# Kernel optimization log

Hardware: AMD Instinct MI355X
Metric: run time of the kernel (lower is better)

The kernel has to match this reference:

```python
import jax, jax.numpy as jnp
import numpy as np

EPS = 1e-5
GROUPS = 32
N_HEADS = 8
HEAD_DIM = 64


def setup_inputs() -> dict:
    key = jax.random.key(0)
    ks = jax.random.split(key, 8)
    b, c, d, w, hs = 2, 512, 16, 16, 16
    ctx_len, ctx_dim = 1024, 768
    inner = N_HEADS * HEAD_DIM  # 512
    return {
        "x": jax.random.normal(ks[0], (b, c, d, w, hs), jnp.float32),
        "context": jax.random.normal(ks[1], (b, ctx_len, ctx_dim), jnp.float32),
        "gamma": jnp.ones((c,), jnp.float32),
        "beta": jnp.zeros((c,), jnp.float32),
        "Wq": jax.random.normal(ks[2], (c, inner), jnp.float32) * (c ** -0.5),
        "Wk": jax.random.normal(ks[3], (ctx_dim, inner), jnp.float32) * (ctx_dim ** -0.5),
        "Wv": jax.random.normal(ks[4], (ctx_dim, inner), jnp.float32) * (ctx_dim ** -0.5),
        "Wo": jax.random.normal(ks[5], (inner, c), jnp.float32) * (inner ** -0.5),
        "bo": jnp.zeros((c,), jnp.float32),
    }


def reference(x, context, gamma, beta, Wq, Wk, Wv, Wo, bo):
    b, c, d, w, hs = x.shape
    n = d * w * hs  # sequence length of voxel tokens
    scale = HEAD_DIM ** -0.5

    # GroupNorm over (channels-in-group, spatial)
    xg = x.reshape(b, GROUPS, -1)
    mu = jnp.mean(xg, axis=-1, keepdims=True)
    var = jnp.mean(jnp.square(xg - mu), axis=-1, keepdims=True)
    xn = (xg - mu) * jax.lax.rsqrt(var + EPS)
    xn = xn.reshape(b, c, n) * gamma[None, :, None] + beta[None, :, None]

    x_seq = jnp.swapaxes(x.reshape(b, c, n), 1, 2)   # [b, n, c] residual
    xn_seq = jnp.swapaxes(xn, 1, 2)                   # [b, n, c]

    q = (xn_seq @ Wq).reshape(b, n, N_HEADS, HEAD_DIM)
    k = (context @ Wk).reshape(b, -1, N_HEADS, HEAD_DIM)
    v = (context @ Wv).reshape(b, -1, N_HEADS, HEAD_DIM)

    attn = jax.nn.softmax(jnp.einsum('bqhd,bkhd->bhqk', q, k) * scale, axis=-1)
    out = jnp.einsum('bhqk,bkhd->bqhd', attn, v).reshape(b, n, N_HEADS * HEAD_DIM)

    out = out @ Wo + bo  # dropout is identity in eval mode
    out = out + x_seq
    return jnp.swapaxes(out, 1, 2).reshape(b, c, d, w, hs)
```

## Files before the change

### kernel.cpp

```cpp
#include <hip/hip_runtime.h>
#include <hip/hip_bf16.h>

#define B 2
#define C 512
#define NTOK 4096
#define GROUPS 32
#define CPG 16
#define CTX 1024
#define CDIM 768
#define NH 8
#define HD 64
#define INNER 512
#define EPS 1e-5f
#define KVBLK 64
#define NCH (CTX / KVBLK)

typedef unsigned short bf16_t;
typedef __attribute__((ext_vector_type(8))) short bf16x8;
typedef __attribute__((ext_vector_type(4))) float f32x4;

__device__ __forceinline__ bf16_t f2b(float f) {
    unsigned u = __float_as_uint(f);
    u += 0x7fffu + ((u >> 16) & 1u);
    return (bf16_t)(u >> 16);
}

__device__ __forceinline__ int swz(int row, int col) {
    return row * 64 + (col ^ ((row & 7) << 3));
}

__global__ __launch_bounds__(256) void gn_partial_kernel(const float* __restrict__ x,
                                                         float2* __restrict__ partials) {
    int blk = blockIdx.x;
    const float* base = x + (size_t)blk * 4096;
    float s = 0.f, ss = 0.f;
    #pragma unroll
    for (int i = 0; i < 4; ++i) {
        float4 v = *(const float4*)&base[(threadIdx.x + i * 256) * 4];
        s += v.x + v.y + v.z + v.w;
        ss += v.x * v.x + v.y * v.y + v.z * v.z + v.w * v.w;
    }
    #pragma unroll
    for (int o = 32; o > 0; o >>= 1) { s += __shfl_xor(s, o); ss += __shfl_xor(ss, o); }
    __shared__ float ls[2][4];
    int wv = threadIdx.x >> 6, ln = threadIdx.x & 63;
    if (ln == 0) { ls[0][wv] = s; ls[1][wv] = ss; }
    __syncthreads();
    if (threadIdx.x == 0) {
        partials[blk] = make_float2(ls[0][0] + ls[0][1] + ls[0][2] + ls[0][3],
                                    ls[1][0] + ls[1][1] + ls[1][2] + ls[1][3]);
    }
}

__global__ __launch_bounds__(64) void gn_finalize_kernel(const float2* __restrict__ partials,
                                                         float* __restrict__ stats) {
    int g = threadIdx.x;
    float s = 0.f, ss = 0.f;
    #pragma unroll
    for (int i = 0; i < 16; ++i) {
        float2 p = partials[g * 16 + i];
        s += p.x; ss += p.y;
    }
    float mu = s / (float)(CPG * NTOK);
    float var = ss / (float)(CPG * NTOK) - mu * mu;
    stats[g] = mu;
    stats[64 + g] = rsqrtf(var + EPS);
}

__global__ __launch_bounds__(256) void gn_apply_kernel(const float* __restrict__ x,
                                                       const float* __restrict__ stats,
                                                       const float* __restrict__ gamma,
                                                       const float* __restrict__ beta,
                                                       bf16_t* __restrict__ xn) {
    __shared__ float tile[32][33];
    int b = blockIdx.z;
    int c0 = blockIdx.y * 32;
    int t0 = blockIdx.x * 32;
    int tt = threadIdx.x & 31, cr = threadIdx.x >> 5;
    #pragma unroll
    for (int i = 0; i < 4; ++i) {
        int c = c0 + cr + 8 * i;
        float mu = stats[b * 32 + (c >> 4)];
        float rs = stats[64 + b * 32 + (c >> 4)];
        float v = x[((size_t)(b * C + c)) * NTOK + t0 + tt];
        tile[cr + 8 * i][tt] = (v - mu) * rs * gamma[c] + beta[c];
    }
    __syncthreads();
    #pragma unroll
    for (int i = 0; i < 4; ++i) {
        int t = t0 + cr + 8 * i;
        int c = c0 + tt;
        xn[((size_t)b * NTOK + t) * C + c] = f2b(tile[tt][cr + 8 * i]);
    }
}

__global__ __launch_bounds__(256) void wcast_kernel(const float* __restrict__ in,
                                                    bf16_t* __restrict__ out,
                                                    int K, int N, int ldo) {
    __shared__ float t[32][33];
    int k0 = blockIdx.x * 32, n0 = blockIdx.y * 32;
    int xx = threadIdx.x & 31, yy = threadIdx.x >> 5;
    #pragma unroll
    for (int i = 0; i < 4; ++i)
        t[yy + 8 * i][xx] = in[(size_t)(k0 + yy + 8 * i) * N + n0 + xx];
    __syncthreads();
    #pragma unroll
    for (int i = 0; i < 4; ++i)
        out[(size_t)(n0 + yy + 8 * i) * ldo + k0 + xx] = f2b(t[xx][yy + 8 * i]);
}

__global__ __launch_bounds__(256) void castctx_kernel(const float* __restrict__ in,
                                                      bf16_t* __restrict__ out) {
    int i = (blockIdx.x * 256 + threadIdx.x) * 4;
    float4 v = *(const float4*)&in[i];
    out[i + 0] = f2b(v.x); out[i + 1] = f2b(v.y);
    out[i + 2] = f2b(v.z); out[i + 3] = f2b(v.w);
}

__global__ __launch_bounds__(256) void gemm_qkv_kernel(
    const bf16_t* __restrict__ A, const bf16_t* __restrict__ Bt,
    bf16_t* __restrict__ outK, bf16_t* __restrict__ outV,
    int K, int seqshift, float oscale, int vtrans) {
    __shared__ __align__(16) bf16_t As[64][40];
    __shared__ __align__(16) bf16_t Bs[64][40];
    const int tid = threadIdx.x;
    const int l = tid & 63, w = tid >> 6;
    const int wr = w >> 1, wc = w & 1;
    const int lg = l >> 4, lr = l & 15;
    const int m0 = blockIdx.x * 64, n0 = blockIdx.y * 64;
    const int rowS = tid >> 2, c8 = (tid & 3) * 8;
    const bf16_t* pa = A  + (size_t)(m0 + rowS) * K + c8;
    const bf16_t* pb = Bt + (size_t)(n0 + rowS) * K + c8;
    f32x4 acc[2][2] = {};
    float4 ra = *(const float4*)pa;
    float4 rb = *(const float4*)pb;
    *(float4*)&As[rowS][c8] = ra;
    *(float4*)&Bs[rowS][c8] = rb;
    for (int k0 = 0; k0 < K; k0 += 32) {
        __syncthreads();
        if (k0 + 32 < K) {
            ra = *(const float4*)(pa + k0 + 32);
            rb = *(const float4*)(pb + k0 + 32);
        }
        bf16x8 af[2], bfm[2];
        af[0]  = *(bf16x8*)&As[wr * 32 + lr][lg * 8];
        af[1]  = *(bf16x8*)&As[wr * 32 + 16 + lr][lg * 8];
        bfm[0] = *(bf16x8*)&Bs[wc * 32 + lr][lg * 8];
        bfm[1] = *(bf16x8*)&Bs[wc * 32 + 16 + lr][lg * 8];
        #pragma unroll
        for (int mi = 0; mi < 2; ++mi)
            #pragma unroll
            for (int ni = 0; ni < 2; ++ni)
                acc[mi][ni] = __builtin_amdgcn_mfma_f32_16x16x32_bf16(af[mi], bfm[ni], acc[mi][ni], 0, 0, 0);
        __syncthreads();
        if (k0 + 32 < K) {
            *(float4*)&As[rowS][c8] = ra;
            *(float4*)&Bs[rowS][c8] = rb;
        }
    }
    const int seqmask = (1 << seqshift) - 1;
    #pragma unroll
    for (int ni = 0; ni < 2; ++ni) {
        int n = n0 + wc * 32 + ni * 16 + lr;
        int nn = n & (INNER - 1);
        int h = nn >> 6, dd = nn & 63;
        bool isV = (n >= INNER);
        #pragma unroll
        for (int mi = 0; mi < 2; ++mi) {
            int mb = m0 + wr * 32 + mi * 16 + lg * 4;
            int bidx = mb >> seqshift, seqb = mb & seqmask;
            if (isV && vtrans) {
                ushort4 pv;
                pv.x = f2b(acc[mi][ni][0] * oscale);
                pv.y = f2b(acc[mi][ni][1] * oscale);
                pv.z = f2b(acc[mi][ni][2] * oscale);
                pv.w = f2b(acc[mi][ni][3] * oscale);
                *(ushort4*)&outV[((size_t)(bidx * NH + h) * HD + dd) * (size_t)(seqmask + 1) + seqb] = pv;
            } else {
                bf16_t* dst = isV ? outV : outK;
                #pragma unroll
                for (int r = 0; r < 4; ++r)
                    dst[(((size_t)(bidx * NH + h) << seqshift) + seqb + r) * HD + dd] =
                        f2b(acc[mi][ni][r] * oscale);
            }
        }
    }
}

__global__ __launch_bounds__(256) void gemm_o_kernel(
    const bf16_t* __restrict__ A, const bf16_t* __restrict__ Bt,
    const float* __restrict__ bo, const float* __restrict__ x,
    float* __restrict__ out) {
    __shared__ __align__(16) bf16_t As[64][40];
    __shared__ __align__(16) bf16_t Bs[64][40];
    const int tid = threadIdx.x;
    const int l = tid & 63, w = tid >> 6;
    const int wr = w >> 1, wc = w & 1;
    const int lg = l >> 4, lr = l & 15;
    const int m0 = blockIdx.x * 64, n0 = blockIdx.y * 64;
    const int rowS = tid >> 2, c8 = (tid & 3) * 8;
    const bf16_t* pa = A  + (size_t)(m0 + rowS) * INNER + c8;
    const bf16_t* pb = Bt + (size_t)(n0 + rowS) * INNER + c8;
    f32x4 acc[2][2] = {};
    float4 ra = *(const float4*)pa;
    float4 rb = *(const float4*)pb;
    *(float4*)&As[rowS][c8] = ra;
    *(float4*)&Bs[rowS][c8] = rb;
    for (int k0 = 0; k0 < INNER; k0 += 32) {
        __syncthreads();
        if (k0 + 32 < INNER) {
            ra = *(const float4*)(pa + k0 + 32);
            rb = *(const float4*)(pb + k0 + 32);
        }
        bf16x8 af[2], bfm[2];
        af[0]  = *(bf16x8*)&As[wr * 32 + lr][lg * 8];
        af[1]  = *(bf16x8*)&As[wr * 32 + 16 + lr][lg * 8];
        bfm[0] = *(bf16x8*)&Bs[wc * 32 + lr][lg * 8];
        bfm[1] = *(bf16x8*)&Bs[wc * 32 + 16 + lr][lg * 8];
        #pragma unroll
        for (int mi = 0; mi < 2; ++mi)
            #pragma unroll
            for (int ni = 0; ni < 2; ++ni)
                acc[mi][ni] = __builtin_amdgcn_mfma_f32_16x16x32_bf16(af[mi], bfm[ni], acc[mi][ni], 0, 0, 0);
        __syncthreads();
        if (k0 + 32 < INNER) {
            *(float4*)&As[rowS][c8] = ra;
            *(float4*)&Bs[rowS][c8] = rb;
        }
    }
    #pragma unroll
    for (int mi = 0; mi < 2; ++mi) {
        int mb = m0 + wr * 32 + mi * 16 + lg * 4;
        int t = mb & (NTOK - 1);
        int bb = mb >> 12;
        #pragma unroll
        for (int ni = 0; ni < 2; ++ni) {
            int cc = n0 + wc * 32 + ni * 16 + lr;
            size_t o = (((size_t)(bb * C + cc)) << 12) + t;
            float4 xr = *(const float4*)&x[o];
            float bias = bo[cc];
            float4 ov;
            ov.x = acc[mi][ni][0] + bias + xr.x;
            ov.y = acc[mi][ni][1] + bias + xr.y;
            ov.z = acc[mi][ni][2] + bias + xr.z;
            ov.w = acc[mi][ni][3] + bias + xr.w;
            *(float4*)&out[o] = ov;
        }
    }
}

__global__ __launch_bounds__(256) void attn_kernel(
    const bf16_t* __restrict__ Q, const bf16_t* __restrict__ Kb,
    const bf16_t* __restrict__ Vt, bf16_t* __restrict__ AO) {
    __shared__ __align__(16) bf16_t Ks[64 * 64];
    __shared__ __align__(16) bf16_t Vs[64 * 64];
    __shared__ __align__(16) bf16_t Ps[4][32 * 64];
    const int tid = threadIdx.x;
    const int l = tid & 63, w = tid >> 6;
    const int lg = l >> 4, lr = l & 15;
    const int bh = blockIdx.x >> 5;
    const int tile = blockIdx.x & 31;
    const int b = bh >> 3, h = bh & 7;
    const int t0 = tile * 128 + w * 32;

    bf16x8 qf[2][2];
    #pragma unroll
    for (int mi = 0; mi < 2; ++mi) {
        const bf16_t* qb = Q + ((size_t)bh * NTOK + t0 + mi * 16 + lr) * HD;
        qf[mi][0] = *(const bf16x8*)&qb[lg * 8];
        qf[mi][1] = *(const bf16x8*)&qb[32 + lg * 8];
    }

    f32x4 acc[2][4] = {};
    float mrow[2][4], lrow[2][4];
    #pragma unroll
    for (int mi = 0; mi < 2; ++mi)
        #pragma unroll
        for (int r = 0; r < 4; ++r) { mrow[mi][r] = -1e30f; lrow[mi][r] = 0.f; }

    const bf16_t* kbase = Kb + (size_t)bh * CTX * HD;
    const bf16_t* vbase = Vt + (size_t)bh * HD * CTX;
    const int srow = tid >> 3, sc8 = (tid & 7) * 8;

    float4 kr0 = *(const float4*)&kbase[(size_t)srow * HD + sc8];
    float4 kr1 = *(const float4*)&kbase[(size_t)(srow + 32) * HD + sc8];
    float4 vr0 = *(const float4*)&vbase[(size_t)srow * CTX + sc8];
    float4 vr1 = *(const float4*)&vbase[(size_t)(srow + 32) * CTX + sc8];
    *(float4*)&Ks[swz(srow, sc8)] = kr0;
    *(float4*)&Ks[swz(srow + 32, sc8)] = kr1;
    *(float4*)&Vs[swz(srow, sc8)] = vr0;
    *(float4*)&Vs[swz(srow + 32, sc8)] = vr1;

    for (int c = 0; c < NCH; ++c) {
        __syncthreads();
        if (c + 1 < NCH) {
            int k1 = (c + 1) * KVBLK;
            kr0 = *(const float4*)&kbase[(size_t)(k1 + srow) * HD + sc8];
            kr1 = *(const float4*)&kbase[(size_t)(k1 + srow + 32) * HD + sc8];
            vr0 = *(const float4*)&vbase[(size_t)srow * CTX + k1 + sc8];
            vr1 = *(const float4*)&vbase[(size_t)(srow + 32) * CTX + k1 + sc8];
        }
        f32x4 sf[2][4] = {};
        #pragma unroll
        for (int ks = 0; ks < 2; ++ks)
            #pragma unroll
            for (int ni = 0; ni < 4; ++ni) {
                bf16x8 kf = *(bf16x8*)&Ks[swz(ni * 16 + lr, ks * 32 + lg * 8)];
                sf[0][ni] = __builtin_amdgcn_mfma_f32_16x16x32_bf16(qf[0][ks], kf, sf[0][ni], 0, 0, 0);
                sf[1][ni] = __builtin_amdgcn_mfma_f32_16x16x32_bf16(qf[1][ks], kf, sf[1][ni], 0, 0, 0);
            }
        #pragma unroll
        for (int mi = 0; mi < 2; ++mi)
            #pragma unroll
            for (int r = 0; r < 4; ++r) {
                float s0 = sf[mi][0][r], s1 = sf[mi][1][r];
                float s2 = sf[mi][2][r], s3 = sf[mi][3][r];
                float cm = fmaxf(fmaxf(s0, s1), fmaxf(s2, s3));
                cm = fmaxf(cm, __shfl_xor(cm, 1));
                cm = fmaxf(cm, __shfl_xor(cm, 2));
                cm = fmaxf(cm, __shfl_xor(cm, 4));
                cm = fmaxf(cm, __shfl_xor(cm, 8));
                float mn = fmaxf(mrow[mi][r], cm);
                float scl = __expf(mrow[mi][r] - mn);
                float p0 = __expf(s0 - mn), p1 = __expf(s1 - mn);
                float p2 = __expf(s2 - mn), p3 = __expf(s3 - mn);
                float rs = p0 + p1 + p2 + p3;
                rs += __shfl_xor(rs, 1); rs += __shfl_xor(rs, 2);
                rs += __shfl_xor(rs, 4); rs += __shfl_xor(rs, 8);
                lrow[mi][r] = lrow[mi][r] * scl + rs;
                mrow[mi][r] = mn;
                #pragma unroll
                for (int ni = 0; ni < 4; ++ni) acc[mi][ni][r] *= scl;
                int prow = mi * 16 + lg * 4 + r;
                Ps[w][swz(prow, 0 * 16 + lr)] = f2b(p0);
                Ps[w][swz(prow, 1 * 16 + lr)] = f2b(p1);
                Ps[w][swz(prow, 2 * 16 + lr)] = f2b(p2);
                Ps[w][swz(prow, 3 * 16 + lr)] = f2b(p3);
            }
        #pragma unroll
        for (int ks = 0; ks < 2; ++ks) {
            bf16x8 pf0 = *(bf16x8*)&Ps[w][swz(lr, ks * 32 + lg * 8)];
            bf16x8 pf1 = *(bf16x8*)&Ps[w][swz(16 + lr, ks * 32 + lg * 8)];
            #pragma unroll
            for (int ni = 0; ni < 4; ++ni) {
                bf16x8 vf = *(bf16x8*)&Vs[swz(ni * 16 + lr, ks * 32 + lg * 8)];
                acc[0][ni] = __builtin_amdgcn_mfma_f32_16x16x32_bf16(pf0, vf, acc[0][ni], 0, 0, 0);
                acc[1][ni] = __builtin_amdgcn_mfma_f32_16x16x32_bf16(pf1, vf, acc[1][ni], 0, 0, 0);
            }
        }
        __syncthreads();
        if (c + 1 < NCH) {
            *(float4*)&Ks[swz(srow, sc8)] = kr0;
            *(float4*)&Ks[swz(srow + 32, sc8)] = kr1;
            *(float4*)&Vs[swz(srow, sc8)] = vr0;
            *(float4*)&Vs[swz(srow + 32, sc8)] = vr1;
        }
    }

    #pragma unroll
    for (int mi = 0; mi < 2; ++mi)
        #pragma unroll
        for (int ni = 0; ni < 4; ++ni)
            #pragma unroll
            for (int r = 0; r < 4; ++r) {
                int t = t0 + mi * 16 + lg * 4 + r;
                AO[((size_t)b * NTOK + t) * INNER + h * HD + ni * 16 + lr] =
                    f2b(acc[mi][ni][r] / lrow[mi][r]);
            }
}

extern "C" void kernel_launch(void* const* d_in, const int* in_sizes, int n_in,
                              void* d_out, int out_size, void* d_ws, size_t ws_size,
                              hipStream_t stream) {
    const float* x       = (const float*)d_in[0];
    const float* context = (const float*)d_in[1];
    const float* gamma   = (const float*)d_in[2];
    const float* beta    = (const float*)d_in[3];
    const float* Wq      = (const float*)d_in[4];
    const float* Wk      = (const float*)d_in[5];
    const float* Wv      = (const float*)d_in[6];
    const float* Wo      = (const float*)d_in[7];
    const float* bo      = (const float*)d_in[8];
    float* out = (float*)d_out;

    char* p = (char*)d_ws;
    float* stats = (float*)p;            p += 1024;
    float2* parts = (float2*)p;          p += 1024 * sizeof(float2);
    bf16_t* xn   = (bf16_t*)p;           p += (size_t)B * NTOK * C * 2;
    bf16_t* ctxb = (bf16_t*)p;           p += (size_t)B * CTX * CDIM * 2;
    bf16_t* Wqt  = (bf16_t*)p;           p += (size_t)INNER * C * 2;
    bf16_t* Wkvt = (bf16_t*)p;           p += (size_t)2 * INNER * CDIM * 2;
    bf16_t* Wot  = (bf16_t*)p;           p += (size_t)C * INNER * 2;
    bf16_t* qb   = (bf16_t*)p;           p += (size_t)B * NH * NTOK * HD * 2;
    bf16_t* kb   = (bf16_t*)p;           p += (size_t)B * NH * CTX * HD * 2;
    bf16_t* vb   = (bf16_t*)p;           p += (size_t)B * NH * CTX * HD * 2;
    bf16_t* ao   = (bf16_t*)p;           p += (size_t)B * NTOK * INNER * 2;

    hipLaunchKernelGGL(gn_partial_kernel, dim3(1024), dim3(256), 0, stream, x, parts);
    hipLaunchKernelGGL(gn_finalize_kernel, dim3(1), dim3(64), 0, stream, parts, stats);
    hipLaunchKernelGGL(gn_apply_kernel, dim3(NTOK / 32, C / 32, B), dim3(256), 0, stream,
                       x, stats, gamma, beta, xn);
    hipLaunchKernelGGL(wcast_kernel, dim3(16, 16), dim3(256), 0, stream, Wq, Wqt, C, INNER, C);
    hipLaunchKernelGGL(wcast_kernel, dim3(24, 16), dim3(256), 0, stream, Wk, Wkvt, CDIM, INNER, CDIM);
    hipLaunchKernelGGL(wcast_kernel, dim3(24, 16), dim3(256), 0, stream,
                       Wv, Wkvt + (size_t)INNER * CDIM, CDIM, INNER, CDIM);
    hipLaunchKernelGGL(wcast_kernel, dim3(16, 16), dim3(256), 0, stream, Wo, Wot, INNER, C, INNER);
    hipLaunchKernelGGL(castctx_kernel, dim3(B * CTX * CDIM / 1024), dim3(256), 0, stream,
                       context, ctxb);
    hipLaunchKernelGGL(gemm_qkv_kernel, dim3(128, 8), dim3(256), 0, stream,
                       xn, Wqt, qb, qb, C, 12, 0.125f, 0);
    hipLaunchKernelGGL(gemm_qkv_kernel, dim3(32, 16), dim3(256), 0, stream,
                       ctxb, Wkvt, kb, vb, CDIM, 10, 1.0f, 1);
    hipLaunchKernelGGL(attn_kernel, dim3(B * NH * (NTOK / 128)), dim3(256), 0, stream,
                       qb, kb, vb, ao);
    hipLaunchKernelGGL(gemm_o_kernel, dim3(128, 8), dim3(256), 0, stream,
                       ao, Wot, bo, x, out);
}
```

Before: 201.8 us.

## Fuse GN finalize, batch weight casts, cast context in GEMM, shrink attention tiles

The GroupNorm finalize step now runs inside the apply kernel, the four weight-cast launches become one launch, and the context fp32→bf16 cast is done inside the K/V GEMM's A-tile load, which drops two launches and an intermediate buffer. The attention kernel is reworked so each wave handles 16 query rows instead of 32, doubling the grid and halving registers and P scratch. Softmax now uses exp2 with log2e folded into the Q scale. The exchange is more redundant K/V tile loading per query and extra conversion work inside the GEMM loop.

```diff
diff --git a/kernel.cpp b/kernel.cpp
--- a/kernel.cpp
+++ b/kernel.cpp
@@ -14,6 +14,7 @@
 #define EPS 1e-5f
 #define KVBLK 64
 #define NCH (CTX / KVBLK)
+#define LOG2E 1.44269504f
 
 typedef unsigned short bf16_t;
 typedef __attribute__((ext_vector_type(8))) short bf16x8;
@@ -23,6 +24,13 @@
     unsigned u = __float_as_uint(f);
     u += 0x7fffu + ((u >> 16) & 1u);
     return (bf16_t)(u >> 16);
+}
+
+__device__ __forceinline__ float4 pack8(const float* v) {
+    union { ushort s[8]; float4 f; } u;
+    #pragma unroll
+    for (int j = 0; j < 8; ++j) u.s[j] = f2b(v[j]);
+    return u.f;
 }
 
 __device__ __forceinline__ int swz(int row, int col) {
@@ -52,38 +60,39 @@
     }
 }
 
-__global__ __launch_bounds__(64) void gn_finalize_kernel(const float2* __restrict__ partials,
-                                                         float* __restrict__ stats) {
-    int g = threadIdx.x;
-    float s = 0.f, ss = 0.f;
-    #pragma unroll
-    for (int i = 0; i < 16; ++i) {
-        float2 p = partials[g * 16 + i];
-        s += p.x; ss += p.y;
-    }
-    float mu = s / (float)(CPG * NTOK);
-    float var = ss / (float)(CPG * NTOK) - mu * mu;
-    stats[g] = mu;
-    stats[64 + g] = rsqrtf(var + EPS);
-}
-
 __global__ __launch_bounds__(256) void gn_apply_kernel(const float* __restrict__ x,
-                                                       const float* __restrict__ stats,
+                                                       const float2* __restrict__ partials,
                                                        const float* __restrict__ gamma,
                                                        const float* __restrict__ beta,
                                                        bf16_t* __restrict__ xn) {
     __shared__ float tile[32][33];
+    __shared__ float gmu[2], grs[2];
     int b = blockIdx.z;
     int c0 = blockIdx.y * 32;
     int t0 = blockIdx.x * 32;
-    int tt = threadIdx.x & 31, cr = threadIdx.x >> 5;
+    int tid = threadIdx.x;
+    if (tid < 32) {
+        int gi = tid >> 4, pi = tid & 15;
+        float2 pp = partials[b * C + c0 + gi * 16 + pi];
+        float s = pp.x, ss = pp.y;
+        #pragma unroll
+        for (int o = 8; o > 0; o >>= 1) { s += __shfl_xor(s, o); ss += __shfl_xor(ss, o); }
+        if (pi == 0) {
+            float mu = s / (float)(CPG * NTOK);
+            float var = ss / (float)(CPG * NTOK) - mu * mu;
+            gmu[gi] = mu;
+            grs[gi] = rsqrtf(var + EPS);
+        }
+    }
+    int tt = tid & 31, cr = tid >> 5;
+    __syncthreads();
     #pragma unroll
     for (int i = 0; i < 4; ++i) {
-        int c = c0 + cr + 8 * i;
-        float mu = stats[b * 32 + (c >> 4)];
-        float rs = stats[64 + b * 32 + (c >> 4)];
+        int co = cr + 8 * i;
+        int c = c0 + co;
+        float mu = gmu[co >> 4], rs = grs[co >> 4];
         float v = x[((size_t)(b * C + c)) * NTOK + t0 + tt];
-        tile[cr + 8 * i][tt] = (v - mu) * rs * gamma[c] + beta[c];
+        tile[co][tt] = (v - mu) * rs * gamma[c] + beta[c];
     }
     __syncthreads();
     #pragma unroll
@@ -94,31 +103,32 @@
     }
 }
 
-__global__ __launch_bounds__(256) void wcast_kernel(const float* __restrict__ in,
-                                                    bf16_t* __restrict__ out,
-                                                    int K, int N, int ldo) {
+__global__ __launch_bounds__(256) void wcast_all_kernel(
+    const float* __restrict__ Wq, const float* __restrict__ Wk,
+    const float* __restrict__ Wv, const float* __restrict__ Wo,
+    bf16_t* __restrict__ Wqt, bf16_t* __restrict__ Wkvt, bf16_t* __restrict__ Wot) {
+    int z = blockIdx.z;
+    const float* in; bf16_t* out; int K;
+    if (z == 0)      { in = Wq; out = Wqt;  K = C; }
+    else if (z == 1) { in = Wk; out = Wkvt; K = CDIM; }
+    else if (z == 2) { in = Wv; out = Wkvt + (size_t)INNER * CDIM; K = CDIM; }
+    else             { in = Wo; out = Wot;  K = INNER; }
+    int k0 = blockIdx.x * 32, n0 = blockIdx.y * 32;
+    if (k0 >= K) return;
     __shared__ float t[32][33];
-    int k0 = blockIdx.x * 32, n0 = blockIdx.y * 32;
     int xx = threadIdx.x & 31, yy = threadIdx.x >> 5;
     #pragma unroll
     for (int i = 0; i < 4; ++i)
-        t[yy + 8 * i][xx] = in[(size_t)(k0 + yy + 8 * i) * N + n0 + xx];
+        t[yy + 8 * i][xx] = in[(size_t)(k0 + yy + 8 * i) * INNER + n0 + xx];
     __syncthreads();
     #pragma unroll
     for (int i = 0; i < 4; ++i)
-        out[(size_t)(n0 + yy + 8 * i) * ldo + k0 + xx] = f2b(t[xx][yy + 8 * i]);
-}
-
-__global__ __launch_bounds__(256) void castctx_kernel(const float* __restrict__ in,
-                                                      bf16_t* __restrict__ out) {
-    int i = (blockIdx.x * 256 + threadIdx.x) * 4;
-    float4 v = *(const float4*)&in[i];
-    out[i + 0] = f2b(v.x); out[i + 1] = f2b(v.y);
-    out[i + 2] = f2b(v.z); out[i + 3] = f2b(v.w);
-}
-
+        out[(size_t)(n0 + yy + 8 * i) * K + k0 + xx] = f2b(t[xx][yy + 8 * i]);
+}
+
+template <int AFP32>
 __global__ __launch_bounds__(256) void gemm_qkv_kernel(
-    const bf16_t* __restrict__ A, const bf16_t* __restrict__ Bt,
+    const void* __restrict__ Av, const bf16_t* __restrict__ Bt,
     bf16_t* __restrict__ outK, bf16_t* __restrict__ outV,
     int K, int seqshift, float oscale, int vtrans) {
     __shared__ __align__(16) bf16_t As[64][40];
@@ -129,17 +139,32 @@
     const int lg = l >> 4, lr = l & 15;
     const int m0 = blockIdx.x * 64, n0 = blockIdx.y * 64;
     const int rowS = tid >> 2, c8 = (tid & 3) * 8;
-    const bf16_t* pa = A  + (size_t)(m0 + rowS) * K + c8;
+    const bf16_t* pa16 = AFP32 ? nullptr : (const bf16_t*)Av + (size_t)(m0 + rowS) * K + c8;
+    const float*  pa32 = AFP32 ? (const float*)Av + (size_t)(m0 + rowS) * K + c8 : nullptr;
     const bf16_t* pb = Bt + (size_t)(n0 + rowS) * K + c8;
     f32x4 acc[2][2] = {};
-    float4 ra = *(const float4*)pa;
-    float4 rb = *(const float4*)pb;
+    float av[8];
+    float4 ra, rb;
+    if (AFP32) {
+        *(float4*)&av[0] = *(const float4*)pa32;
+        *(float4*)&av[4] = *(const float4*)(pa32 + 4);
+        ra = pack8(av);
+    } else {
+        ra = *(const float4*)pa16;
+    }
+    rb = *(const float4*)pb;
     *(float4*)&As[rowS][c8] = ra;
     *(float4*)&Bs[rowS][c8] = rb;
     for (int k0 = 0; k0 < K; k0 += 32) {
         __syncthreads();
         if (k0 + 32 < K) {
-            ra = *(const float4*)(pa + k0 + 32);
+            if (AFP32) {
+                *(float4*)&av[0] = *(const float4*)(pa32 + k0 + 32);
+                *(float4*)&av[4] = *(const float4*)(pa32 + k0 + 36);
+                ra = pack8(av);
+            } else {
+                ra = *(const float4*)(pa16 + k0 + 32);
+            }
             rb = *(const float4*)(pb + k0 + 32);
         }
         bf16x8 af[2], bfm[2];
@@ -254,29 +279,24 @@
     const bf16_t* __restrict__ Vt, bf16_t* __restrict__ AO) {
     __shared__ __align__(16) bf16_t Ks[64 * 64];
     __shared__ __align__(16) bf16_t Vs[64 * 64];
-    __shared__ __align__(16) bf16_t Ps[4][32 * 64];
+    __shared__ __align__(16) bf16_t Ps[4][16 * 64];
     const int tid = threadIdx.x;
     const int l = tid & 63, w = tid >> 6;
     const int lg = l >> 4, lr = l & 15;
-    const int bh = blockIdx.x >> 5;
-    const int tile = blockIdx.x & 31;
+    const int bh = blockIdx.x >> 6;
+    const int tile = blockIdx.x & 63;
     const int b = bh >> 3, h = bh & 7;
-    const int t0 = tile * 128 + w * 32;
-
-    bf16x8 qf[2][2];
-    #pragma unroll
-    for (int mi = 0; mi < 2; ++mi) {
-        const bf16_t* qb = Q + ((size_t)bh * NTOK + t0 + mi * 16 + lr) * HD;
-        qf[mi][0] = *(const bf16x8*)&qb[lg * 8];
-        qf[mi][1] = *(const bf16x8*)&qb[32 + lg * 8];
-    }
-
-    f32x4 acc[2][4] = {};
-    float mrow[2][4], lrow[2][4];
-    #pragma unroll
-    for (int mi = 0; mi < 2; ++mi)
-        #pragma unroll
-        for (int r = 0; r < 4; ++r) { mrow[mi][r] = -1e30f; lrow[mi][r] = 0.f; }
+    const int t0 = tile * 64 + w * 16;
+
+    const bf16_t* qbase = Q + ((size_t)bh * NTOK + t0 + lr) * HD;
+    bf16x8 qf[2];
+    qf[0] = *(const bf16x8*)&qbase[lg * 8];
+    qf[1] = *(const bf16x8*)&qbase[32 + lg * 8];
+
+    f32x4 acc[4] = {};
+    float mrow[4], lrow[4];
+    #pragma unroll
+    for (int r = 0; r < 4; ++r) { mrow[r] = -1e30f; lrow[r] = 0.f; }
 
     const bf16_t* kbase = Kb + (size_t)bh * CTX * HD;
     const bf16_t* vbase = Vt + (size_t)bh * HD * CTX;
@@ -300,52 +320,49 @@
             vr0 = *(const float4*)&vbase[(size_t)srow * CTX + k1 + sc8];
             vr1 = *(const float4*)&vbase[(size_t)(srow + 32) * CTX + k1 + sc8];
         }
-        f32x4 sf[2][4] = {};
+        f32x4 sf[4] = {};
         #pragma unroll
         for (int ks = 0; ks < 2; ++ks)
             #pragma unroll
             for (int ni = 0; ni < 4; ++ni) {
                 bf16x8 kf = *(bf16x8*)&Ks[swz(ni * 16 + lr, ks * 32 + lg * 8)];
-                sf[0][ni] = __builtin_amdgcn_mfma_f32_16x16x32_bf16(qf[0][ks], kf, sf[0][ni], 0, 0, 0);
-                sf[1][ni] = __builtin_amdgcn_mfma_f32_16x16x32_bf16(qf[1][ks], kf, sf[1][ni], 0, 0, 0);
+                sf[ni] = __builtin_amdgcn_mfma_f32_16x16x32_bf16(qf[ks], kf, sf[ni], 0, 0, 0);
             }
         #pragma unroll
-        for (int mi = 0; mi < 2; ++mi)
+        for (int r = 0; r < 4; ++r) {
+            float s0 = sf[0][r], s1 = sf[1][r];
+            float s2 = sf[2][r], s3 = sf[3][r];
+            float cm = fmaxf(fmaxf(s0, s1), fmaxf(s2, s3));
+            cm = fmaxf(cm, __shfl_xor(cm, 1));
+            cm = fmaxf(cm, __shfl_xor(cm, 2));
+            cm = fmaxf(cm, __shfl_xor(cm, 4));
+            cm = fmaxf(cm, __shfl_xor(cm, 8));
+            float mn = fmaxf(mrow[r], cm);
+            float scl = __builtin_amdgcn_exp2f(mrow[r] - mn);
+            float p0 = __builtin_amdgcn_exp2f(s0 - mn);
+            float p1 = __builtin_amdgcn_exp2f(s1 - mn);
+            float p2 = __builtin_amdgcn_exp2f(s2 - mn);
+            float p3 = __builtin_amdgcn_exp2f(s3 - mn);
+            float rs = p0 + p1 + p2 + p3;
+            rs += __shfl_xor(rs, 1); rs += __shfl_xor(rs, 2);
+            rs += __shfl_xor(rs, 4); rs += __shfl_xor(rs, 8);
+            lrow[r] = lrow[r] * scl + rs;
+            mrow[r] = mn;
             #pragma unroll
-            for (int r = 0; r < 4; ++r) {
-                float s0 = sf[mi][0][r], s1 = sf[mi][1][r];
-                float s2 = sf[mi][2][r], s3 = sf[mi][3][r];
-                float cm = fmaxf(fmaxf(s0, s1), fmaxf(s2, s3));
-                cm = fmaxf(cm, __shfl_xor(cm, 1));
-                cm = fmaxf(cm, __shfl_xor(cm, 2));
-                cm = fmaxf(cm, __shfl_xor(cm, 4));
-                cm = fmaxf(cm, __shfl_xor(cm, 8));
-                float mn = fmaxf(mrow[mi][r], cm);
-                float scl = __expf(mrow[mi][r] - mn);
-                float p0 = __expf(s0 - mn), p1 = __expf(s1 - mn);
-                float p2 = __expf(s2 - mn), p3 = __expf(s3 - mn);
-                float rs = p0 + p1 + p2 + p3;
-                rs += __shfl_xor(rs, 1); rs += __shfl_xor(rs, 2);
-                rs += __shfl_xor(rs, 4); rs += __shfl_xor(rs, 8);
-                lrow[mi][r] = lrow[mi][r] * scl + rs;
-                mrow[mi][r] = mn;
-                #pragma unroll
-                for (int ni = 0; ni < 4; ++ni) acc[mi][ni][r] *= scl;
-                int prow = mi * 16 + lg * 4 + r;
-                Ps[w][swz(prow, 0 * 16 + lr)] = f2b(p0);
-                Ps[w][swz(prow, 1 * 16 + lr)] = f2b(p1);
-                Ps[w][swz(prow, 2 * 16 + lr)] = f2b(p2);
-                Ps[w][swz(prow, 3 * 16 + lr)] = f2b(p3);
-            }
+            for (int ni = 0; ni < 4; ++ni) acc[ni][r] *= scl;
+            int prow = lg * 4 + r;
+            Ps[w][swz(prow, 0 * 16 + lr)] = f2b(p0);
+            Ps[w][swz(prow, 1 * 16 + lr)] = f2b(p1);
+            Ps[w][swz(prow, 2 * 16 + lr)] = f2b(p2);
+            Ps[w][swz(prow, 3 * 16 + lr)] = f2b(p3);
+        }
         #pragma unroll
         for (int ks = 0; ks < 2; ++ks) {
-            bf16x8 pf0 = *(bf16x8*)&Ps[w][swz(lr, ks * 32 + lg * 8)];
-            bf16x8 pf1 = *(bf16x8*)&Ps[w][swz(16 + lr, ks * 32 + lg * 8)];
+            bf16x8 pf = *(bf16x8*)&Ps[w][swz(lr, ks * 32 + lg * 8)];
             #pragma unroll
             for (int ni = 0; ni < 4; ++ni) {
                 bf16x8 vf = *(bf16x8*)&Vs[swz(ni * 16 + lr, ks * 32 + lg * 8)];
-                acc[0][ni] = __builtin_amdgcn_mfma_f32_16x16x32_bf16(pf0, vf, acc[0][ni], 0, 0, 0);
-                acc[1][ni] = __builtin_amdgcn_mfma_f32_16x16x32_bf16(pf1, vf, acc[1][ni], 0, 0, 0);
+                acc[ni] = __builtin_amdgcn_mfma_f32_16x16x32_bf16(pf, vf, acc[ni], 0, 0, 0);
             }
         }
         __syncthreads();
@@ -358,15 +375,13 @@
     }
 
     #pragma unroll
-    for (int mi = 0; mi < 2; ++mi)
-        #pragma unroll
-        for (int ni = 0; ni < 4; ++ni)
-            #pragma unroll
-            for (int r = 0; r < 4; ++r) {
-                int t = t0 + mi * 16 + lg * 4 + r;
-                AO[((size_t)b * NTOK + t) * INNER + h * HD + ni * 16 + lr] =
-                    f2b(acc[mi][ni][r] / lrow[mi][r]);
-            }
+    for (int ni = 0; ni < 4; ++ni)
+        #pragma unroll
+        for (int r = 0; r < 4; ++r) {
+            int t = t0 + lg * 4 + r;
+            AO[((size_t)b * NTOK + t) * INNER + h * HD + ni * 16 + lr] =
+                f2b(acc[ni][r] / lrow[r]);
+        }
 }
 
 extern "C" void kernel_launch(void* const* d_in, const int* in_sizes, int n_in,
@@ -384,10 +399,8 @@
     float* out = (float*)d_out;
 
     char* p = (char*)d_ws;
-    float* stats = (float*)p;            p += 1024;
     float2* parts = (float2*)p;          p += 1024 * sizeof(float2);
     bf16_t* xn   = (bf16_t*)p;           p += (size_t)B * NTOK * C * 2;
-    bf16_t* ctxb = (bf16_t*)p;           p += (size_t)B * CTX * CDIM * 2;
     bf16_t* Wqt  = (bf16_t*)p;           p += (size_t)INNER * C * 2;
     bf16_t* Wkvt = (bf16_t*)p;           p += (size_t)2 * INNER * CDIM * 2;
     bf16_t* Wot  = (bf16_t*)p;           p += (size_t)C * INNER * 2;
@@ -396,22 +409,16 @@
     bf16_t* vb   = (bf16_t*)p;           p += (size_t)B * NH * CTX * HD * 2;
     bf16_t* ao   = (bf16_t*)p;           p += (size_t)B * NTOK * INNER * 2;
 
-    hipLaunchKernelGGL(gn_partial_kernel, dim3(1024), dim3(256), 0, stream, x, parts);
-    hipLaunchKernelGGL(gn_finalize_kernel, dim3(1), dim3(64), 0, stream, parts, stats);
+    hipLaunchKernelGGL(gn_partial_kernel, dim3(B * C), dim3(256), 0, stream, x, parts);
     hipLaunchKernelGGL(gn_apply_kernel, dim3(NTOK / 32, C / 32, B), dim3(256), 0, stream,
-                       x, stats, gamma, beta, xn);
-    hipLaunchKernelGGL(wcast_kernel, dim3(16, 16), dim3(256), 0, stream, Wq, Wqt, C, INNER, C);
-    hipLaunchKernelGGL(wcast_kernel, dim3(24, 16), dim3(256), 0, stream, Wk, Wkvt, CDIM, INNER, CDIM);
-    hipLaunchKernelGGL(wcast_kernel, dim3(24, 16), dim3(256), 0, stream,
-                       Wv, Wkvt + (size_t)INNER * CDIM, CDIM, INNER, CDIM);
-    hipLaunchKernelGGL(wcast_kernel, dim3(16, 16), dim3(256), 0, stream, Wo, Wot, INNER, C, INNER);
-    hipLaunchKernelGGL(castctx_kernel, dim3(B * CTX * CDIM / 1024), dim3(256), 0, stream,
-                       context, ctxb);
-    hipLaunchKernelGGL(gemm_qkv_kernel, dim3(128, 8), dim3(256), 0, stream,
-                       xn, Wqt, qb, qb, C, 12, 0.125f, 0);
-    hipLaunchKernelGGL(gemm_qkv_kernel, dim3(32, 16), dim3(256), 0, stream,
-                       ctxb, Wkvt, kb, vb, CDIM, 10, 1.0f, 1);
-    hipLaunchKernelGGL(attn_kernel, dim3(B * NH * (NTOK / 128)), dim3(256), 0, stream,
+                       x, parts, gamma, beta, xn);
+    hipLaunchKernelGGL(wcast_all_kernel, dim3(24, 16, 4), dim3(256), 0, stream,
+                       Wq, Wk, Wv, Wo, Wqt, Wkvt, Wot);
+    hipLaunchKernelGGL((gemm_qkv_kernel<0>), dim3(128, 8), dim3(256), 0, stream,
+                       (const void*)xn, Wqt, qb, qb, C, 12, 0.125f * LOG2E, 0);
+    hipLaunchKernelGGL((gemm_qkv_kernel<1>), dim3(32, 16), dim3(256), 0, stream,
+                       (const void*)context, Wkvt, kb, vb, CDIM, 10, 1.0f, 1);
+    hipLaunchKernelGGL(attn_kernel, dim3(B * NH * (NTOK / 64)), dim3(256), 0, stream,
                        qb, kb, vb, ao);
     hipLaunchKernelGGL(gemm_o_kernel, dim3(128, 8), dim3(256), 0, stream,
                        ao, Wot, bo, x, out);
```

Result: faster. 194.7 us (-3.5%).
